# Kernel tuning notes

Measured on AMD Instinct MI355X. Metric: run time of the kernel, lower is better.

Reference implementation:

```python
import jax, jax.numpy as jnp
import numpy as np
from jax import lax

BN_EPS = 1e-5


def _spatial_gate(x, w, g, b, m, v):
    # x: [N, C, H, W]; ChannelPool -> [N, 2, H, W]; 7x7 conv -> [N,1,H,W]; BN (eval); sigmoid gate
    comp = jnp.stack([jnp.max(x, axis=1), jnp.mean(x, axis=1)], axis=1)
    o = lax.conv_general_dilated(comp, w, (1, 1), [(3, 3), (3, 3)],
                                 dimension_numbers=('NCHW', 'OIHW', 'NCHW'))
    o = (o - m[None, :, None, None]) * lax.rsqrt(v + BN_EPS)[None, :, None, None] \
        * g[None, :, None, None] + b[None, :, None, None]
    s = jax.nn.sigmoid(o)
    return x * s


def _eca_sort(x, w_eca):
    # global avg pool -> sort channels desc -> 1D conv over sorted seq -> sigmoid -> unsort -> gate
    y = jnp.mean(x, axis=(2, 3))               # [N, C]
    order = jnp.argsort(-y, axis=1)            # descending sort indices
    rank = jnp.argsort(order, axis=1)          # inverse permutation
    ys = jnp.take_along_axis(y, order, axis=1)  # sorted descending
    k = w_eca.shape[-1]
    p = k // 2
    o = lax.conv_general_dilated(ys[:, None, :], w_eca, (1,), [(p, p)],
                                 dimension_numbers=('NCH', 'OIH', 'NCH'))[:, 0, :]
    sig = jax.nn.sigmoid(o)
    yr = jnp.take_along_axis(sig, rank, axis=1)  # reorder back per original index_select(rank)
    return x * yr[:, :, None, None]


def setup_inputs() -> dict:
    key = jax.random.key(0)
    ks = jax.random.split(key, 6)
    N, C, H, W = 32, 256, 56, 56
    inp = {
        'x': jax.random.normal(ks[0], (N, C, H, W), dtype=jnp.float32),
        'weight': jax.random.normal(ks[1], (1,), dtype=jnp.float32),
        'w_h': jax.random.normal(ks[2], (1, 2, 7, 7), dtype=jnp.float32) * 0.1,
        'g_h': jnp.ones((1,), jnp.float32), 'b_h': jnp.zeros((1,), jnp.float32),
        'm_h': jnp.zeros((1,), jnp.float32), 'v_h': jnp.ones((1,), jnp.float32),
        'w_w': jax.random.normal(ks[3], (1, 2, 7, 7), dtype=jnp.float32) * 0.1,
        'g_w': jnp.ones((1,), jnp.float32), 'b_w': jnp.zeros((1,), jnp.float32),
        'm_w': jnp.zeros((1,), jnp.float32), 'v_w': jnp.ones((1,), jnp.float32),
        'w_s': jax.random.normal(ks[4], (1, 2, 7, 7), dtype=jnp.float32) * 0.1,
        'g_s': jnp.ones((1,), jnp.float32), 'b_s': jnp.zeros((1,), jnp.float32),
        'm_s': jnp.zeros((1,), jnp.float32), 'v_s': jnp.ones((1,), jnp.float32),
        'w_eca': jax.random.normal(ks[5], (1, 1, 5), dtype=jnp.float32) * 0.3,
    }
    return inp


def reference(x, weight, w_h, g_h, b_h, m_h, v_h, w_w, g_w, b_w, m_w, v_w,
              w_s, g_s, b_s, m_s, v_s, w_eca):
    # branch 1: gate over H-as-channel (permute 0,2,1,3)
    xh = jnp.transpose(x, (0, 2, 1, 3))
    x11 = jnp.transpose(_spatial_gate(xh, w_h, g_h, b_h, m_h, v_h), (0, 2, 1, 3))
    # branch 2: gate over W-as-channel (permute 0,3,2,1)
    xw = jnp.transpose(x, (0, 3, 2, 1))
    x21 = jnp.transpose(_spatial_gate(xw, w_w, g_w, b_w, m_w, v_w), (0, 3, 2, 1))
    # branch 3: eca with sort/unsort
    x31 = _eca_sort(x, w_eca)
    # branch 4: plain spatial gate
    xo = _spatial_gate(x, w_s, g_s, b_s, m_s, v_s)
    return 0.23779 * xo + 0.24695 * x11 + 0.24365 * x21 + 0.27173 * x31
```

## Files before the change

kernel.cpp:

```cpp
#include <hip/hip_runtime.h>
#include <math.h>

#define N_ 32
#define C_ 256
#define H_ 56
#define W_ 56
#define HW_ (H_*W_)
#define CHW_ (C_*HW_)
#define NHW_ (N_*HW_)
#define NCW_ (N_*C_*W_)
#define NHC_ (N_*H_*C_)
#define BN_EPS_ 1e-5f

#define TLD 60
#define NB_PL 2048
#define NB_CP 392

__global__ __launch_bounds__(256) void pools_k(
        const float* __restrict__ x,
        float* __restrict__ maxC, float* __restrict__ meanC,
        float* __restrict__ maxH, float* __restrict__ meanH,
        float* __restrict__ maxW, float* __restrict__ meanW,
        float* __restrict__ y) {
    __shared__ float smem[4 * 28 * TLD];
    int b = blockIdx.x;
    int tid = threadIdx.x;
    int wave = tid >> 6, lane = tid & 63;
    const float4* x4 = (const float4*)x;
    if (b < NB_PL) {
        float* tile = &smem[wave * 28 * TLD];
        int pb = b * 4 + wave;
        int n = pb >> 8, c = pb & 255;
        size_t pbase = (size_t)pb * (HW_ / 4);
        float cmx = -INFINITY, csm = 0.f;
        #pragma unroll
        for (int s = 0; s < 2; ++s) {
            #pragma unroll
            for (int i = 0; i < 6; ++i) {
                int j = i * 64 + lane;
                float4 v = x4[pbase + s * 392 + j];
                int hl = j / 14, w4 = j - hl * 14;
                float* d = &tile[hl * TLD + w4 * 4];
                d[0] = v.x; d[1] = v.y; d[2] = v.z; d[3] = v.w;
            }
            if (lane < 8) {
                int j = 384 + lane;
                float4 v = x4[pbase + s * 392 + j];
                int hl = j / 14, w4 = j - hl * 14;
                float* d = &tile[hl * TLD + w4 * 4];
                d[0] = v.x; d[1] = v.y; d[2] = v.z; d[3] = v.w;
            }
            __syncthreads();
            if (lane < W_) {
                #pragma unroll 7
                for (int hl = 0; hl < 28; ++hl) {
                    float v = tile[hl * TLD + lane];
                    cmx = fmaxf(cmx, v); csm += v;
                }
            }
            if (lane < 28) {
                int h = s * 28 + lane;
                const float4* r = (const float4*)&tile[lane * TLD];
                float4 m4 = make_float4(-INFINITY, -INFINITY, -INFINITY, -INFINITY);
                float4 s4 = make_float4(0.f, 0.f, 0.f, 0.f);
                #pragma unroll
                for (int k = 0; k < 14; ++k) {
                    float4 v = r[k];
                    m4.x = fmaxf(m4.x, v.x); m4.y = fmaxf(m4.y, v.y);
                    m4.z = fmaxf(m4.z, v.z); m4.w = fmaxf(m4.w, v.w);
                    s4.x += v.x; s4.y += v.y; s4.z += v.z; s4.w += v.w;
                }
                int o = (n * H_ + h) * C_ + c;
                maxW[o] = fmaxf(fmaxf(m4.x, m4.y), fmaxf(m4.z, m4.w));
                meanW[o] = (s4.x + s4.y + s4.z + s4.w) * (1.f / W_);
            }
            __syncthreads();
        }
        if (lane < W_) {
            int o = (n * C_ + c) * W_ + lane;
            maxH[o] = cmx;
            meanH[o] = csm * (1.f / H_);
        }
        float tot = csm;
        #pragma unroll
        for (int m = 32; m >= 1; m >>= 1) tot += __shfl_xor(tot, m);
        if (lane == 0) y[n * C_ + c] = tot * (1.f / HW_);
    } else {
        float4* smx = (float4*)smem;
        float4* ssm = smx + 256;
        int bb = b - NB_PL;
        int q = bb * 64 + lane;
        int n = q / (HW_ / 4);
        int hw4 = q - n * (HW_ / 4);
        size_t base = (size_t)n * (CHW_ / 4) + hw4 + (size_t)(wave * 64) * (HW_ / 4);
        float4 mx = make_float4(-INFINITY, -INFINITY, -INFINITY, -INFINITY);
        float4 sm = make_float4(0.f, 0.f, 0.f, 0.f);
        #pragma unroll 8
        for (int i = 0; i < 64; ++i) {
            float4 v = x4[base + (size_t)i * (HW_ / 4)];
            mx.x = fmaxf(mx.x, v.x); mx.y = fmaxf(mx.y, v.y);
            mx.z = fmaxf(mx.z, v.z); mx.w = fmaxf(mx.w, v.w);
            sm.x += v.x; sm.y += v.y; sm.z += v.z; sm.w += v.w;
        }
        smx[wave * 64 + lane] = mx;
        ssm[wave * 64 + lane] = sm;
        __syncthreads();
        if (tid < 64) {
            float4 m = smx[tid];
            #pragma unroll
            for (int j = 1; j < 4; ++j) {
                float4 v = smx[j * 64 + tid];
                m.x = fmaxf(m.x, v.x); m.y = fmaxf(m.y, v.y);
                m.z = fmaxf(m.z, v.z); m.w = fmaxf(m.w, v.w);
            }
            ((float4*)maxC)[bb * 64 + tid] = m;
        } else if (tid < 128) {
            int t2 = tid - 64;
            float4 s = ssm[t2];
            #pragma unroll
            for (int j = 1; j < 4; ++j) {
                float4 v = ssm[j * 64 + t2];
                s.x += v.x; s.y += v.y; s.z += v.z; s.w += v.w;
            }
            s.x *= (1.f / C_); s.y *= (1.f / C_); s.z *= (1.f / C_); s.w *= (1.f / C_);
            ((float4*)meanC)[bb * 64 + t2] = s;
        }
    }
}

template <int R, int Cc>
__device__ __forceinline__ void conv7_part(int t, const float* __restrict__ p0,
                                           const float* __restrict__ p1,
                                           const float* __restrict__ wt,
                                           float g, float bb, float m, float v,
                                           float* __restrict__ out) {
    const int per = R * Cc;
    int n = t / per;
    int r2 = t - n * per;
    int i = r2 / Cc, j = r2 - i * Cc;
    const float* b0 = p0 + (size_t)n * per;
    const float* b1 = p1 + (size_t)n * per;
    float acc = 0.f;
    #pragma unroll
    for (int ki = 0; ki < 7; ++ki) {
        int ii = i + ki - 3;
        if (ii < 0 || ii >= R) continue;
        #pragma unroll
        for (int kj = 0; kj < 7; ++kj) {
            int jj = j + kj - 3;
            if (jj < 0 || jj >= Cc) continue;
            int idx = ii * Cc + jj;
            acc += b0[idx] * wt[ki * 7 + kj] + b1[idx] * wt[49 + ki * 7 + kj];
        }
    }
    float o = (acc - m) * rsqrtf(v + BN_EPS_) * g + bb;
    out[t] = 1.f / (1.f + expf(-o));
}

#define NB_SS (NHW_ / 256)
#define NB_SH (NCW_ / 256)
#define NB_SW (NHC_ / 256)

__global__ __launch_bounds__(256) void conv_eca_k(
        const float* __restrict__ maxC, const float* __restrict__ meanC,
        const float* __restrict__ maxH, const float* __restrict__ meanH,
        const float* __restrict__ maxW, const float* __restrict__ meanW,
        const float* __restrict__ w_s, const float* __restrict__ g_s,
        const float* __restrict__ b_s, const float* __restrict__ m_s,
        const float* __restrict__ v_s,
        const float* __restrict__ w_h, const float* __restrict__ g_h,
        const float* __restrict__ b_h, const float* __restrict__ m_h,
        const float* __restrict__ v_h,
        const float* __restrict__ w_w, const float* __restrict__ g_w,
        const float* __restrict__ b_w, const float* __restrict__ m_w,
        const float* __restrict__ v_w,
        const float* __restrict__ y, const float* __restrict__ w_eca,
        float* __restrict__ s_s, float* __restrict__ s_h, float* __restrict__ s_w,
        float* __restrict__ gate) {
    __shared__ float sv[C_];
    __shared__ int si[C_];
    int b = blockIdx.x;
    int tid = threadIdx.x;
    if (b < NB_SS) {
        conv7_part<H_, W_>(b * 256 + tid, maxC, meanC, w_s, g_s[0], b_s[0], m_s[0],
                           v_s[0], s_s);
    } else if (b < NB_SS + NB_SH) {
        conv7_part<C_, W_>((b - NB_SS) * 256 + tid, maxH, meanH, w_h, g_h[0], b_h[0],
                           m_h[0], v_h[0], s_h);
    } else if (b < NB_SS + NB_SH + NB_SW) {
        conv7_part<H_, C_>((b - NB_SS - NB_SH) * 256 + tid, maxW, meanW, w_w, g_w[0],
                           b_w[0], m_w[0], v_w[0], s_w);
    } else {
        int n = b - (NB_SS + NB_SH + NB_SW);
        sv[tid] = y[n * C_ + tid];
        si[tid] = tid;
        __syncthreads();
        for (int k = 2; k <= C_; k <<= 1) {
            for (int j = k >> 1; j > 0; j >>= 1) {
                int ixj = tid ^ j;
                if (ixj > tid) {
                    float v1 = sv[tid], v2 = sv[ixj];
                    int i1 = si[tid], i2 = si[ixj];
                    bool before = (v1 > v2) || (v1 == v2 && i1 < i2);
                    bool dir = ((tid & k) == 0);
                    if (dir ? !before : before) {
                        sv[tid] = v2; sv[ixj] = v1;
                        si[tid] = i2; si[ixj] = i1;
                    }
                }
                __syncthreads();
            }
        }
        float o = 0.f;
        #pragma unroll
        for (int j = 0; j < 5; ++j) {
            int p = tid + j - 2;
            if (p >= 0 && p < C_) o += sv[p] * w_eca[j];
        }
        gate[n * C_ + si[tid]] = 1.f / (1.f + expf(-o));
    }
}

__global__ __launch_bounds__(256) void apply_k(
        const float* __restrict__ x, const float* __restrict__ s_s,
        const float* __restrict__ s_h, const float* __restrict__ s_w,
        const float* __restrict__ gate, float* __restrict__ out) {
    int t = blockIdx.x * 256 + threadIdx.x;
    int f = t * 4;
    int n = f / CHW_;
    int rem = f - n * CHW_;
    int c = rem / HW_;
    int hw = rem - c * HW_;
    int h = hw / W_;
    int w = hw - h * W_;
    float4 xv = ((const float4*)x)[t];
    float4 s4 = *(const float4*)(s_s + (size_t)n * HW_ + hw);
    float4 h4 = *(const float4*)(s_h + ((size_t)n * C_ + c) * W_ + w);
    float sw = s_w[((size_t)n * H_ + h) * C_ + c];
    float ge = gate[n * C_ + c];
    float base = 0.24365f * sw + 0.27173f * ge;
    float4 o;
    o.x = xv.x * (0.23779f * s4.x + 0.24695f * h4.x + base);
    o.y = xv.y * (0.23779f * s4.y + 0.24695f * h4.y + base);
    o.z = xv.z * (0.23779f * s4.z + 0.24695f * h4.z + base);
    o.w = xv.w * (0.23779f * s4.w + 0.24695f * h4.w + base);
    ((float4*)out)[t] = o;
}

extern "C" void kernel_launch(void* const* d_in, const int* in_sizes, int n_in,
                              void* d_out, int out_size, void* d_ws, size_t ws_size,
                              hipStream_t stream) {
    const float* x     = (const float*)d_in[0];
    const float* w_h   = (const float*)d_in[2];
    const float* g_h   = (const float*)d_in[3];
    const float* b_h   = (const float*)d_in[4];
    const float* m_h   = (const float*)d_in[5];
    const float* v_h   = (const float*)d_in[6];
    const float* w_w   = (const float*)d_in[7];
    const float* g_w   = (const float*)d_in[8];
    const float* b_w   = (const float*)d_in[9];
    const float* m_w   = (const float*)d_in[10];
    const float* v_w   = (const float*)d_in[11];
    const float* w_s   = (const float*)d_in[12];
    const float* g_s   = (const float*)d_in[13];
    const float* b_s   = (const float*)d_in[14];
    const float* m_s   = (const float*)d_in[15];
    const float* v_s   = (const float*)d_in[16];
    const float* w_eca = (const float*)d_in[17];
    float* out = (float*)d_out;

    float* ws    = (float*)d_ws;
    float* maxC  = ws;
    float* meanC = maxC  + NHW_;
    float* maxH  = meanC + NHW_;
    float* meanH = maxH  + NCW_;
    float* maxW  = meanH + NCW_;
    float* meanW = maxW  + NHC_;
    float* s_s   = meanW + NHC_;
    float* s_h   = s_s   + NHW_;
    float* s_w   = s_h   + NCW_;
    float* yv    = s_w   + NHC_;
    float* gate  = yv    + N_ * C_;

    pools_k<<<NB_PL + NB_CP, 256, 0, stream>>>(x, maxC, meanC, maxH, meanH,
                                               maxW, meanW, yv);

    int conv_blocks = NB_SS + NB_SH + NB_SW + N_;
    conv_eca_k<<<conv_blocks, 256, 0, stream>>>(maxC, meanC, maxH, meanH, maxW, meanW,
                                                w_s, g_s, b_s, m_s, v_s,
                                                w_h, g_h, b_h, m_h, v_h,
                                                w_w, g_w, b_w, m_w, v_w,
                                                yv, w_eca, s_s, s_h, s_w, gate);

    apply_k<<<(N_ * CHW_ / 4) / 256, 256, 0, stream>>>(x, s_s, s_h, s_w, gate, out);
}
```

Measured before the change: 103.4 us.

## Replace LDS tile transpose in pools with register/shuffle reductions; reorder block roles

The per-plane pooling path no longer stages a 28x60 tile in shared memory. Each wave now loads its plane into registers, 14 float4 per lane, and computes the H-pool, W-pool and global-mean reductions with cross-lane shuffles. This removes the LDS writes and reads and the block-wide barriers. The channel-pool blocks are moved first in the grid and their loop is unrolled further. apply_k now processes two float4 per thread with half as many blocks. The costs are higher register pressure from the 14-element buffer and idle lanes, since only 14 of every 16 lanes are active.

```diff
diff --git a/kernel.cpp b/kernel.cpp
--- a/kernel.cpp
+++ b/kernel.cpp
@@ -6,15 +6,15 @@
 #define H_ 56
 #define W_ 56
 #define HW_ (H_*W_)
+#define HW4_ (HW_/4)
 #define CHW_ (C_*HW_)
 #define NHW_ (N_*HW_)
 #define NCW_ (N_*C_*W_)
 #define NHC_ (N_*H_*C_)
 #define BN_EPS_ 1e-5f
 
-#define TLD 60
+#define NB_CP 392
 #define NB_PL 2048
-#define NB_CP 392
 
 __global__ __launch_bounds__(256) void pools_k(
         const float* __restrict__ x,
@@ -22,109 +22,107 @@
         float* __restrict__ maxH, float* __restrict__ meanH,
         float* __restrict__ maxW, float* __restrict__ meanW,
         float* __restrict__ y) {
-    __shared__ float smem[4 * 28 * TLD];
+    __shared__ float4 smx[4][64];
+    __shared__ float4 ssm[4][64];
     int b = blockIdx.x;
     int tid = threadIdx.x;
     int wave = tid >> 6, lane = tid & 63;
     const float4* x4 = (const float4*)x;
-    if (b < NB_PL) {
-        float* tile = &smem[wave * 28 * TLD];
-        int pb = b * 4 + wave;
-        int n = pb >> 8, c = pb & 255;
-        size_t pbase = (size_t)pb * (HW_ / 4);
-        float cmx = -INFINITY, csm = 0.f;
-        #pragma unroll
-        for (int s = 0; s < 2; ++s) {
-            #pragma unroll
-            for (int i = 0; i < 6; ++i) {
-                int j = i * 64 + lane;
-                float4 v = x4[pbase + s * 392 + j];
-                int hl = j / 14, w4 = j - hl * 14;
-                float* d = &tile[hl * TLD + w4 * 4];
-                d[0] = v.x; d[1] = v.y; d[2] = v.z; d[3] = v.w;
-            }
-            if (lane < 8) {
-                int j = 384 + lane;
-                float4 v = x4[pbase + s * 392 + j];
-                int hl = j / 14, w4 = j - hl * 14;
-                float* d = &tile[hl * TLD + w4 * 4];
-                d[0] = v.x; d[1] = v.y; d[2] = v.z; d[3] = v.w;
-            }
-            __syncthreads();
-            if (lane < W_) {
-                #pragma unroll 7
-                for (int hl = 0; hl < 28; ++hl) {
-                    float v = tile[hl * TLD + lane];
-                    cmx = fmaxf(cmx, v); csm += v;
-                }
-            }
-            if (lane < 28) {
-                int h = s * 28 + lane;
-                const float4* r = (const float4*)&tile[lane * TLD];
-                float4 m4 = make_float4(-INFINITY, -INFINITY, -INFINITY, -INFINITY);
-                float4 s4 = make_float4(0.f, 0.f, 0.f, 0.f);
-                #pragma unroll
-                for (int k = 0; k < 14; ++k) {
-                    float4 v = r[k];
-                    m4.x = fmaxf(m4.x, v.x); m4.y = fmaxf(m4.y, v.y);
-                    m4.z = fmaxf(m4.z, v.z); m4.w = fmaxf(m4.w, v.w);
-                    s4.x += v.x; s4.y += v.y; s4.z += v.z; s4.w += v.w;
-                }
-                int o = (n * H_ + h) * C_ + c;
-                maxW[o] = fmaxf(fmaxf(m4.x, m4.y), fmaxf(m4.z, m4.w));
-                meanW[o] = (s4.x + s4.y + s4.z + s4.w) * (1.f / W_);
-            }
-            __syncthreads();
-        }
-        if (lane < W_) {
-            int o = (n * C_ + c) * W_ + lane;
-            maxH[o] = cmx;
-            meanH[o] = csm * (1.f / H_);
-        }
-        float tot = csm;
-        #pragma unroll
-        for (int m = 32; m >= 1; m >>= 1) tot += __shfl_xor(tot, m);
-        if (lane == 0) y[n * C_ + c] = tot * (1.f / HW_);
-    } else {
-        float4* smx = (float4*)smem;
-        float4* ssm = smx + 256;
-        int bb = b - NB_PL;
-        int q = bb * 64 + lane;
-        int n = q / (HW_ / 4);
-        int hw4 = q - n * (HW_ / 4);
-        size_t base = (size_t)n * (CHW_ / 4) + hw4 + (size_t)(wave * 64) * (HW_ / 4);
+    if (b < NB_CP) {
+        int q = b * 64 + lane;
+        int n = q / HW4_;
+        int hw4 = q - n * HW4_;
+        size_t base = (size_t)n * (CHW_ / 4) + hw4 + (size_t)(wave * 64) * HW4_;
         float4 mx = make_float4(-INFINITY, -INFINITY, -INFINITY, -INFINITY);
         float4 sm = make_float4(0.f, 0.f, 0.f, 0.f);
-        #pragma unroll 8
+        #pragma unroll 16
         for (int i = 0; i < 64; ++i) {
-            float4 v = x4[base + (size_t)i * (HW_ / 4)];
+            float4 v = x4[base + (size_t)i * HW4_];
             mx.x = fmaxf(mx.x, v.x); mx.y = fmaxf(mx.y, v.y);
             mx.z = fmaxf(mx.z, v.z); mx.w = fmaxf(mx.w, v.w);
             sm.x += v.x; sm.y += v.y; sm.z += v.z; sm.w += v.w;
         }
-        smx[wave * 64 + lane] = mx;
-        ssm[wave * 64 + lane] = sm;
+        smx[wave][lane] = mx;
+        ssm[wave][lane] = sm;
         __syncthreads();
         if (tid < 64) {
-            float4 m = smx[tid];
+            float4 m = smx[0][tid];
             #pragma unroll
             for (int j = 1; j < 4; ++j) {
-                float4 v = smx[j * 64 + tid];
+                float4 v = smx[j][tid];
                 m.x = fmaxf(m.x, v.x); m.y = fmaxf(m.y, v.y);
                 m.z = fmaxf(m.z, v.z); m.w = fmaxf(m.w, v.w);
             }
-            ((float4*)maxC)[bb * 64 + tid] = m;
+            ((float4*)maxC)[b * 64 + tid] = m;
         } else if (tid < 128) {
             int t2 = tid - 64;
-            float4 s = ssm[t2];
+            float4 s = ssm[0][t2];
             #pragma unroll
             for (int j = 1; j < 4; ++j) {
-                float4 v = ssm[j * 64 + t2];
+                float4 v = ssm[j][t2];
                 s.x += v.x; s.y += v.y; s.z += v.z; s.w += v.w;
             }
             s.x *= (1.f / C_); s.y *= (1.f / C_); s.z *= (1.f / C_); s.w *= (1.f / C_);
-            ((float4*)meanC)[bb * 64 + t2] = s;
-        }
+            ((float4*)meanC)[b * 64 + t2] = s;
+        }
+    } else {
+        int pb = (b - NB_CP) * 4 + wave;
+        int n = pb >> 8, c = pb & 255;
+        size_t pbase = (size_t)pb * HW4_;
+        int g = lane >> 4, q = lane & 15;
+        bool act = q < 14;
+        float4 v[14];
+        size_t base = pbase + g * 14 + q;
+        #pragma unroll
+        for (int t = 0; t < 14; ++t) {
+            if (act) v[t] = x4[base + 56 * t];
+        }
+        float4 cmx = make_float4(-INFINITY, -INFINITY, -INFINITY, -INFINITY);
+        float4 csm = make_float4(0.f, 0.f, 0.f, 0.f);
+        #pragma unroll
+        for (int t = 0; t < 14; ++t) {
+            cmx.x = fmaxf(cmx.x, v[t].x); cmx.y = fmaxf(cmx.y, v[t].y);
+            cmx.z = fmaxf(cmx.z, v[t].z); cmx.w = fmaxf(cmx.w, v[t].w);
+            csm.x += v[t].x; csm.y += v[t].y; csm.z += v[t].z; csm.w += v[t].w;
+        }
+        #pragma unroll
+        for (int t = 0; t < 14; ++t) {
+            float rmx = act ? fmaxf(fmaxf(v[t].x, v[t].y), fmaxf(v[t].z, v[t].w))
+                            : -INFINITY;
+            float rsm = act ? (v[t].x + v[t].y + v[t].z + v[t].w) : 0.f;
+            #pragma unroll
+            for (int off = 8; off >= 1; off >>= 1) {
+                rmx = fmaxf(rmx, __shfl_xor(rmx, off));
+                rsm += __shfl_xor(rsm, off);
+            }
+            if (q == 0) {
+                int h = 4 * t + g;
+                int o = (n * H_ + h) * C_ + c;
+                maxW[o] = rmx;
+                meanW[o] = rsm * (1.f / W_);
+            }
+        }
+        #pragma unroll
+        for (int off = 16; off <= 32; off <<= 1) {
+            cmx.x = fmaxf(cmx.x, __shfl_xor(cmx.x, off));
+            cmx.y = fmaxf(cmx.y, __shfl_xor(cmx.y, off));
+            cmx.z = fmaxf(cmx.z, __shfl_xor(cmx.z, off));
+            cmx.w = fmaxf(cmx.w, __shfl_xor(cmx.w, off));
+            csm.x += __shfl_xor(csm.x, off);
+            csm.y += __shfl_xor(csm.y, off);
+            csm.z += __shfl_xor(csm.z, off);
+            csm.w += __shfl_xor(csm.w, off);
+        }
+        if (g == 0 && act) {
+            ((float4*)maxH)[(n * C_ + c) * 14 + q] = cmx;
+            float4 mh = make_float4(csm.x * (1.f / H_), csm.y * (1.f / H_),
+                                    csm.z * (1.f / H_), csm.w * (1.f / H_));
+            ((float4*)meanH)[(n * C_ + c) * 14 + q] = mh;
+        }
+        float sq = act ? (csm.x + csm.y + csm.z + csm.w) : 0.f;
+        #pragma unroll
+        for (int off = 8; off >= 1; off >>= 1) sq += __shfl_xor(sq, off);
+        if (lane == 0) y[n * C_ + c] = sq * (1.f / HW_);
     }
 }
 
@@ -225,26 +223,30 @@
         const float* __restrict__ x, const float* __restrict__ s_s,
         const float* __restrict__ s_h, const float* __restrict__ s_w,
         const float* __restrict__ gate, float* __restrict__ out) {
-    int t = blockIdx.x * 256 + threadIdx.x;
-    int f = t * 4;
-    int n = f / CHW_;
-    int rem = f - n * CHW_;
-    int c = rem / HW_;
-    int hw = rem - c * HW_;
-    int h = hw / W_;
-    int w = hw - h * W_;
-    float4 xv = ((const float4*)x)[t];
-    float4 s4 = *(const float4*)(s_s + (size_t)n * HW_ + hw);
-    float4 h4 = *(const float4*)(s_h + ((size_t)n * C_ + c) * W_ + w);
-    float sw = s_w[((size_t)n * H_ + h) * C_ + c];
-    float ge = gate[n * C_ + c];
-    float base = 0.24365f * sw + 0.27173f * ge;
-    float4 o;
-    o.x = xv.x * (0.23779f * s4.x + 0.24695f * h4.x + base);
-    o.y = xv.y * (0.23779f * s4.y + 0.24695f * h4.y + base);
-    o.z = xv.z * (0.23779f * s4.z + 0.24695f * h4.z + base);
-    o.w = xv.w * (0.23779f * s4.w + 0.24695f * h4.w + base);
-    ((float4*)out)[t] = o;
+    int t0 = blockIdx.x * 512 + threadIdx.x;
+    #pragma unroll
+    for (int r = 0; r < 2; ++r) {
+        int t = t0 + r * 256;
+        int f = t * 4;
+        int n = f / CHW_;
+        int rem = f - n * CHW_;
+        int c = rem / HW_;
+        int hw = rem - c * HW_;
+        int h = hw / W_;
+        int w = hw - h * W_;
+        float4 xv = ((const float4*)x)[t];
+        float4 s4 = *(const float4*)(s_s + (size_t)n * HW_ + hw);
+        float4 h4 = *(const float4*)(s_h + ((size_t)n * C_ + c) * W_ + w);
+        float sw = s_w[((size_t)n * H_ + h) * C_ + c];
+        float ge = gate[n * C_ + c];
+        float base = 0.24365f * sw + 0.27173f * ge;
+        float4 o;
+        o.x = xv.x * (0.23779f * s4.x + 0.24695f * h4.x + base);
+        o.y = xv.y * (0.23779f * s4.y + 0.24695f * h4.y + base);
+        o.z = xv.z * (0.23779f * s4.z + 0.24695f * h4.z + base);
+        o.w = xv.w * (0.23779f * s4.w + 0.24695f * h4.w + base);
+        ((float4*)out)[t] = o;
+    }
 }
 
 extern "C" void kernel_launch(void* const* d_in, const int* in_sizes, int n_in,
@@ -282,7 +284,7 @@
     float* yv    = s_w   + NHC_;
     float* gate  = yv    + N_ * C_;
 
-    pools_k<<<NB_PL + NB_CP, 256, 0, stream>>>(x, maxC, meanC, maxH, meanH,
+    pools_k<<<NB_CP + NB_PL, 256, 0, stream>>>(x, maxC, meanC, maxH, meanH,
                                                maxW, meanW, yv);
 
     int conv_blocks = NB_SS + NB_SH + NB_SW + N_;
@@ -292,5 +294,5 @@
                                                 w_w, g_w, b_w, m_w, v_w,
                                                 yv, w_eca, s_s, s_h, s_w, gate);
 
-    apply_k<<<(N_ * CHW_ / 4) / 256, 256, 0, stream>>>(x, s_s, s_h, s_w, gate, out);
-}
+    apply_k<<<(N_ * CHW_ / 4) / 512, 256, 0, stream>>>(x, s_s, s_h, s_w, gate, out);
+}
```

Measured after the change: 106.3 us. +2.7%, slower.

## Double-buffer plane pooling across 8 planes per block, rebalance pool blocks

Applied to the files above, without the earlier changes.

The plane-pooling path now gives each 256-thread block 8 consecutive (n,c) planes instead of one plane per wave. It prefetches the next plane into registers while the current one is reduced from a double-buffered shared tile, and splits the column and row reductions across threads with shuffles. The channel-pool path switches to 32-lane groups over 8 channel chunks, which doubles its block count. The apply kernel now handles two float4s per thread. This aims to hide global load latency and cut per-plane block overhead, at the cost of fewer blocks in the plane phase and more barriers per block.

```diff
diff --git a/kernel.cpp b/kernel.cpp
--- a/kernel.cpp
+++ b/kernel.cpp
@@ -6,6 +6,7 @@
 #define H_ 56
 #define W_ 56
 #define HW_ (H_*W_)
+#define HW4_ (HW_/4)
 #define CHW_ (C_*HW_)
 #define NHW_ (N_*HW_)
 #define NCW_ (N_*C_*W_)
@@ -13,8 +14,14 @@
 #define BN_EPS_ 1e-5f
 
 #define TLD 60
-#define NB_PL 2048
-#define NB_CP 392
+#define PLANES_PER_BLK 8
+#define NB_PL 1024
+#define NB_CP 784
+
+#define SM_BUF1 3360
+#define SM_CPMX 6720
+#define SM_CPSM (6720 + 224)
+#define SM_TOT  (6720 + 448)
 
 __global__ __launch_bounds__(256) void pools_k(
         const float* __restrict__ x,
@@ -22,108 +29,145 @@
         float* __restrict__ maxH, float* __restrict__ meanH,
         float* __restrict__ maxW, float* __restrict__ meanW,
         float* __restrict__ y) {
-    __shared__ float smem[4 * 28 * TLD];
+    __shared__ float smem[SM_TOT];
     int b = blockIdx.x;
     int tid = threadIdx.x;
-    int wave = tid >> 6, lane = tid & 63;
     const float4* x4 = (const float4*)x;
     if (b < NB_PL) {
-        float* tile = &smem[wave * 28 * TLD];
-        int pb = b * 4 + wave;
-        int n = pb >> 8, c = pb & 255;
-        size_t pbase = (size_t)pb * (HW_ / 4);
-        float cmx = -INFINITY, csm = 0.f;
-        #pragma unroll
-        for (int s = 0; s < 2; ++s) {
-            #pragma unroll
-            for (int i = 0; i < 6; ++i) {
-                int j = i * 64 + lane;
-                float4 v = x4[pbase + s * 392 + j];
-                int hl = j / 14, w4 = j - hl * 14;
-                float* d = &tile[hl * TLD + w4 * 4];
-                d[0] = v.x; d[1] = v.y; d[2] = v.z; d[3] = v.w;
-            }
-            if (lane < 8) {
-                int j = 384 + lane;
-                float4 v = x4[pbase + s * 392 + j];
-                int hl = j / 14, w4 = j - hl * 14;
-                float* d = &tile[hl * TLD + w4 * 4];
-                d[0] = v.x; d[1] = v.y; d[2] = v.z; d[3] = v.w;
+        float* buf0 = smem;
+        float* buf1 = smem + SM_BUF1;
+        float* cpmx = smem + SM_CPMX;
+        float* cpsm = smem + SM_CPSM;
+        int pb0 = b * PLANES_PER_BLK;
+        float4 r0, r1, r2, r3;
+        int row0 = tid / 14,          col0 = (tid % 14) * 4;
+        int row1 = (tid + 256) / 14,  col1 = ((tid + 256) % 14) * 4;
+        int row2 = (tid + 512) / 14,  col2 = ((tid + 512) % 14) * 4;
+        int row3 = (tid + 768) / 14,  col3 = ((tid + 768) % 14) * 4;
+        {
+            size_t base = (size_t)pb0 * HW4_;
+            r0 = x4[base + tid];
+            r1 = x4[base + 256 + tid];
+            r2 = x4[base + 512 + tid];
+            if (tid < 16) r3 = x4[base + 768 + tid];
+        }
+        {
+            float* d = buf0;
+            *(float4*)&d[row0 * TLD + col0] = r0;
+            *(float4*)&d[row1 * TLD + col1] = r1;
+            *(float4*)&d[row2 * TLD + col2] = r2;
+            if (tid < 16) *(float4*)&d[row3 * TLD + col3] = r3;
+        }
+        __syncthreads();
+        for (int k = 0; k < PLANES_PER_BLK; ++k) {
+            float* cur = (k & 1) ? buf1 : buf0;
+            float* nxt = (k & 1) ? buf0 : buf1;
+            int pb = pb0 + k;
+            int n = pb >> 8, c = pb & 255;
+            if (k < PLANES_PER_BLK - 1) {
+                size_t base = (size_t)(pb + 1) * HW4_;
+                r0 = x4[base + tid];
+                r1 = x4[base + 256 + tid];
+                r2 = x4[base + 512 + tid];
+                if (tid < 16) r3 = x4[base + 768 + tid];
+            }
+            if (tid < 224) {
+                int w = tid % 56, hq = tid / 56;
+                const float* base = &cur[(hq * 14) * TLD + w];
+                float mx = -INFINITY, sm = 0.f;
+                #pragma unroll
+                for (int hh = 0; hh < 14; ++hh) {
+                    float v = base[hh * TLD];
+                    mx = fmaxf(mx, v); sm += v;
+                }
+                cpmx[hq * 56 + w] = mx;
+                cpsm[hq * 56 + w] = sm;
             }
             __syncthreads();
-            if (lane < W_) {
-                #pragma unroll 7
-                for (int hl = 0; hl < 28; ++hl) {
-                    float v = tile[hl * TLD + lane];
-                    cmx = fmaxf(cmx, v); csm += v;
-                }
-            }
-            if (lane < 28) {
-                int h = s * 28 + lane;
-                const float4* r = (const float4*)&tile[lane * TLD];
-                float4 m4 = make_float4(-INFINITY, -INFINITY, -INFINITY, -INFINITY);
-                float4 s4 = make_float4(0.f, 0.f, 0.f, 0.f);
+            float colsum = 0.f;
+            if (tid < 56) {
+                float mx = cpmx[tid], sm = cpsm[tid];
                 #pragma unroll
-                for (int k = 0; k < 14; ++k) {
-                    float4 v = r[k];
-                    m4.x = fmaxf(m4.x, v.x); m4.y = fmaxf(m4.y, v.y);
-                    m4.z = fmaxf(m4.z, v.z); m4.w = fmaxf(m4.w, v.w);
-                    s4.x += v.x; s4.y += v.y; s4.z += v.z; s4.w += v.w;
-                }
-                int o = (n * H_ + h) * C_ + c;
-                maxW[o] = fmaxf(fmaxf(m4.x, m4.y), fmaxf(m4.z, m4.w));
-                meanW[o] = (s4.x + s4.y + s4.z + s4.w) * (1.f / W_);
+                for (int j = 1; j < 4; ++j) {
+                    mx = fmaxf(mx, cpmx[j * 56 + tid]);
+                    sm += cpsm[j * 56 + tid];
+                }
+                int o = (n * C_ + c) * W_ + tid;
+                maxH[o] = mx;
+                meanH[o] = sm * (1.f / H_);
+                colsum = sm;
+            }
+            if (tid < 64) {
+                float t = colsum;
+                #pragma unroll
+                for (int off = 32; off >= 1; off >>= 1) t += __shfl_xor(t, off);
+                if (tid == 0) y[n * C_ + c] = t * (1.f / HW_);
+            }
+            if (tid < 224) {
+                int h = tid >> 2, kq = tid & 3;
+                const float* base = &cur[h * TLD + kq * 14];
+                float mx = -INFINITY, sm = 0.f;
+                #pragma unroll
+                for (int kk = 0; kk < 14; ++kk) {
+                    float v = base[kk];
+                    mx = fmaxf(mx, v); sm += v;
+                }
+                mx = fmaxf(mx, __shfl_xor(mx, 1)); sm += __shfl_xor(sm, 1);
+                mx = fmaxf(mx, __shfl_xor(mx, 2)); sm += __shfl_xor(sm, 2);
+                if (kq == 0) {
+                    int o = (n * H_ + h) * C_ + c;
+                    maxW[o] = mx;
+                    meanW[o] = sm * (1.f / W_);
+                }
+            }
+            if (k < PLANES_PER_BLK - 1) {
+                *(float4*)&nxt[row0 * TLD + col0] = r0;
+                *(float4*)&nxt[row1 * TLD + col1] = r1;
+                *(float4*)&nxt[row2 * TLD + col2] = r2;
+                if (tid < 16) *(float4*)&nxt[row3 * TLD + col3] = r3;
             }
             __syncthreads();
         }
-        if (lane < W_) {
-            int o = (n * C_ + c) * W_ + lane;
-            maxH[o] = cmx;
-            meanH[o] = csm * (1.f / H_);
-        }
-        float tot = csm;
-        #pragma unroll
-        for (int m = 32; m >= 1; m >>= 1) tot += __shfl_xor(tot, m);
-        if (lane == 0) y[n * C_ + c] = tot * (1.f / HW_);
     } else {
         float4* smx = (float4*)smem;
         float4* ssm = smx + 256;
         int bb = b - NB_PL;
-        int q = bb * 64 + lane;
-        int n = q / (HW_ / 4);
-        int hw4 = q - n * (HW_ / 4);
-        size_t base = (size_t)n * (CHW_ / 4) + hw4 + (size_t)(wave * 64) * (HW_ / 4);
+        int g = tid >> 5, qi = tid & 31;
+        int q = bb * 32 + qi;
+        int n = q / HW4_;
+        int hw4 = q - n * HW4_;
+        size_t base = (size_t)n * (CHW_ / 4) + hw4 + (size_t)(g * 32) * HW4_;
         float4 mx = make_float4(-INFINITY, -INFINITY, -INFINITY, -INFINITY);
         float4 sm = make_float4(0.f, 0.f, 0.f, 0.f);
-        #pragma unroll 8
-        for (int i = 0; i < 64; ++i) {
-            float4 v = x4[base + (size_t)i * (HW_ / 4)];
+        #pragma unroll 16
+        for (int i = 0; i < 32; ++i) {
+            float4 v = x4[base + (size_t)i * HW4_];
             mx.x = fmaxf(mx.x, v.x); mx.y = fmaxf(mx.y, v.y);
             mx.z = fmaxf(mx.z, v.z); mx.w = fmaxf(mx.w, v.w);
             sm.x += v.x; sm.y += v.y; sm.z += v.z; sm.w += v.w;
         }
-        smx[wave * 64 + lane] = mx;
-        ssm[wave * 64 + lane] = sm;
+        smx[g * 32 + qi] = mx;
+        ssm[g * 32 + qi] = sm;
         __syncthreads();
-        if (tid < 64) {
+        if (tid < 32) {
             float4 m = smx[tid];
             #pragma unroll
-            for (int j = 1; j < 4; ++j) {
-                float4 v = smx[j * 64 + tid];
+            for (int j = 1; j < 8; ++j) {
+                float4 v = smx[j * 32 + tid];
                 m.x = fmaxf(m.x, v.x); m.y = fmaxf(m.y, v.y);
                 m.z = fmaxf(m.z, v.z); m.w = fmaxf(m.w, v.w);
             }
-            ((float4*)maxC)[bb * 64 + tid] = m;
-        } else if (tid < 128) {
-            int t2 = tid - 64;
+            ((float4*)maxC)[bb * 32 + tid] = m;
+        } else if (tid < 64) {
+            int t2 = tid - 32;
             float4 s = ssm[t2];
             #pragma unroll
-            for (int j = 1; j < 4; ++j) {
-                float4 v = ssm[j * 64 + t2];
+            for (int j = 1; j < 8; ++j) {
+                float4 v = ssm[j * 32 + t2];
                 s.x += v.x; s.y += v.y; s.z += v.z; s.w += v.w;
             }
             s.x *= (1.f / C_); s.y *= (1.f / C_); s.z *= (1.f / C_); s.w *= (1.f / C_);
-            ((float4*)meanC)[bb * 64 + t2] = s;
+            ((float4*)meanC)[bb * 32 + t2] = s;
         }
     }
 }
@@ -225,26 +269,30 @@
         const float* __restrict__ x, const float* __restrict__ s_s,
         const float* __restrict__ s_h, const float* __restrict__ s_w,
         const float* __restrict__ gate, float* __restrict__ out) {
-    int t = blockIdx.x * 256 + threadIdx.x;
-    int f = t * 4;
-    int n = f / CHW_;
-    int rem = f - n * CHW_;
-    int c = rem / HW_;
-    int hw = rem - c * HW_;
-    int h = hw / W_;
-    int w = hw - h * W_;
-    float4 xv = ((const float4*)x)[t];
-    float4 s4 = *(const float4*)(s_s + (size_t)n * HW_ + hw);
-    float4 h4 = *(const float4*)(s_h + ((size_t)n * C_ + c) * W_ + w);
-    float sw = s_w[((size_t)n * H_ + h) * C_ + c];
-    float ge = gate[n * C_ + c];
-    float base = 0.24365f * sw + 0.27173f * ge;
-    float4 o;
-    o.x = xv.x * (0.23779f * s4.x + 0.24695f * h4.x + base);
-    o.y = xv.y * (0.23779f * s4.y + 0.24695f * h4.y + base);
-    o.z = xv.z * (0.23779f * s4.z + 0.24695f * h4.z + base);
-    o.w = xv.w * (0.23779f * s4.w + 0.24695f * h4.w + base);
-    ((float4*)out)[t] = o;
+    int t0 = blockIdx.x * 512 + threadIdx.x;
+    #pragma unroll
+    for (int r = 0; r < 2; ++r) {
+        int t = t0 + r * 256;
+        int f = t * 4;
+        int n = f / CHW_;
+        int rem = f - n * CHW_;
+        int c = rem / HW_;
+        int hw = rem - c * HW_;
+        int h = hw / W_;
+        int w = hw - h * W_;
+        float4 xv = ((const float4*)x)[t];
+        float4 s4 = *(const float4*)(s_s + (size_t)n * HW_ + hw);
+        float4 h4 = *(const float4*)(s_h + ((size_t)n * C_ + c) * W_ + w);
+        float sw = s_w[((size_t)n * H_ + h) * C_ + c];
+        float ge = gate[n * C_ + c];
+        float base = 0.24365f * sw + 0.27173f * ge;
+        float4 o;
+        o.x = xv.x * (0.23779f * s4.x + 0.24695f * h4.x + base);
+        o.y = xv.y * (0.23779f * s4.y + 0.24695f * h4.y + base);
+        o.z = xv.z * (0.23779f * s4.z + 0.24695f * h4.z + base);
+        o.w = xv.w * (0.23779f * s4.w + 0.24695f * h4.w + base);
+        ((float4*)out)[t] = o;
+    }
 }
 
 extern "C" void kernel_launch(void* const* d_in, const int* in_sizes, int n_in,
@@ -292,5 +340,5 @@
                                                 w_w, g_w, b_w, m_w, v_w,
                                                 yv, w_eca, s_s, s_h, s_w, gate);
 
-    apply_k<<<(N_ * CHW_ / 4) / 256, 256, 0, stream>>>(x, s_s, s_h, s_w, gate, out);
-}
+    apply_k<<<(N_ * CHW_ / 4) / 512, 256, 0, stream>>>(x, s_s, s_h, s_w, gate, out);
+}
```

Measured after the change: 110.6 us. +6.9%, slower.
